# Kernel tuning notes

Measured on AMD Instinct MI355X. Metric: run time of the kernel, lower is better.

The kernel has to match this reference:

```python
import jax, jax.numpy as jnp
import numpy as np

EPS = 1e-5


def gcn_conv(x, W, b, src, dst, ew, num_nodes):
    """GCNConv with add_self_loops=True, symmetric normalization (PyG default)."""
    # degree at destination, self-loop weight 1.0 included implicitly
    deg = jax.ops.segment_sum(ew, dst, num_segments=num_nodes) + 1.0  # [N]
    dinv = jax.lax.rsqrt(deg)                                         # deg >= 1
    norm = dinv[src] * ew * dinv[dst]                                 # [E]
    h = x @ W                                                         # [N, F]
    msg = norm[:, None] * h[src]                                      # [E, F]
    agg = jax.ops.segment_sum(msg, dst, num_segments=num_nodes)       # [N, F]
    # self-loop contribution: dinv[i] * 1 * dinv[i] = 1/deg[i]
    agg = agg + h * (1.0 / deg)[:, None]
    return agg + b


def batchnorm(h, gamma, beta):
    mean = jnp.mean(h, axis=0)
    var = jnp.mean(jnp.square(h - mean), axis=0)  # biased, training-mode stats
    return (h - mean) * jax.lax.rsqrt(var + EPS) * gamma + beta


def setup_inputs() -> dict:
    key = jax.random.key(0)
    ks = jax.random.split(key, 8)
    N, E, F = 50000, 800000, 64
    x = jax.random.normal(ks[0], (N, F), dtype=jnp.float32)
    edge_index = jax.random.randint(ks[1], (2, E), 0, N, dtype=jnp.int64)
    edge_weight = jax.random.uniform(ks[2], (E,), dtype=jnp.float32)
    s = 1.0 / np.sqrt(F)
    W1 = jax.random.uniform(ks[3], (F, F), jnp.float32, -s, s)
    b1 = jnp.zeros((F,), jnp.float32)
    W2 = jax.random.uniform(ks[4], (F, F), jnp.float32, -s, s)
    b2 = jnp.zeros((F,), jnp.float32)
    gamma1 = jnp.ones((F,), jnp.float32)
    beta1 = jnp.zeros((F,), jnp.float32)
    gamma2 = jnp.ones((F,), jnp.float32)
    beta2 = jnp.zeros((F,), jnp.float32)
    return {"x": x, "edge_index": edge_index, "edge_weight": edge_weight,
            "W1": W1, "b1": b1, "gamma1": gamma1, "beta1": beta1,
            "W2": W2, "b2": b2, "gamma2": gamma2, "beta2": beta2}


def reference(x, edge_index, edge_weight, W1, b1, gamma1, beta1, W2, b2, gamma2, beta2):
    N = x.shape[0]
    src, dst = edge_index[0], edge_index[1]
    identity = x
    out = gcn_conv(x, W1, b1, src, dst, edge_weight, N)
    out = jax.nn.relu(batchnorm(out, gamma1, beta1))
    out = gcn_conv(out, W2, b2, src, dst, edge_weight, N)
    out = batchnorm(out, gamma2, beta2)
    out = out + identity  # residual: num_input_features == hidden_dim
    return jax.nn.relu(out)
```

## Files before the change

### kernel.cpp

```cpp
#include <hip/hip_runtime.h>
#include <math.h>

#define FEAT 64
#define BN_EPS 1e-5f
#define BN_REPS 64
#define CNT_REPS 4

__device__ __forceinline__ int edge_idx(const void* p, int is64, long long i) {
    return is64 ? (int)((const long long*)p)[i] : ((const int*)p)[i];
}

__device__ __forceinline__ float4 f4fma(float a, float4 b, float4 c) {
    return make_float4(fmaf(a, b.x, c.x), fmaf(a, b.y, c.y),
                       fmaf(a, b.z, c.z), fmaf(a, b.w, c.w));
}

__device__ __forceinline__ unsigned bf16rtne(float f) {
    unsigned u = __float_as_uint(f);
    return (u + 0x7fffu + ((u >> 16) & 1u)) >> 16;
}
__device__ __forceinline__ unsigned packbf2(float a, float b) {
    return bf16rtne(a) | (bf16rtne(b) << 16);
}
__device__ __forceinline__ float4 unpackbf4(uint2 r) {
    return make_float4(__uint_as_float(r.x << 16),
                       __uint_as_float(r.x & 0xffff0000u),
                       __uint_as_float(r.y << 16),
                       __uint_as_float(r.y & 0xffff0000u));
}

__global__ __launch_bounds__(256) void init_kernel(
    const unsigned* __restrict__ w, int* __restrict__ flag,
    int* __restrict__ cnt, float* __restrict__ parts, int N4) {
    int i = blockIdx.x * 256 + threadIdx.x;
    if (i < N4) cnt[i] = 0;
    if (blockIdx.x < 64) parts[blockIdx.x * 256 + threadIdx.x] = 0.0f;
    if (blockIdx.x == 0 && threadIdx.x < 64) {
        unsigned long long ok = __ballot(w[2 * threadIdx.x + 1] == 0u);
        if (threadIdx.x == 0) *flag = (ok == ~0ull);
    }
}

__global__ __launch_bounds__(256) void fused_count_gemm1_kernel(
    const void* __restrict__ ei, const int* __restrict__ flag,
    int* __restrict__ cnt, int* __restrict__ seq, int E,
    const float* __restrict__ x, const float* __restrict__ W1,
    uint2* __restrict__ out_bf, int N, int nc) {
    __shared__ float4 Ws4[64][16];
    __shared__ float xs[64][65];
    int tid = threadIdx.x;

    if ((int)blockIdx.x < nc) {
        int is64 = *flag;
        int T = nc * 256;
        int i = blockIdx.x * 256 + tid;
#pragma unroll
        for (int u = 0; u < 8; ++u) {
            int e = i + u * T;
            if (e < E) {
                int dst = edge_idx(ei, is64, (long long)E + e);
                seq[e] = atomicAdd(&cnt[(e & 3) * N + dst], 1);
            }
        }
        return;
    }

    int gb = blockIdx.x - nc;
    const float4* W4 = (const float4*)W1;
    for (int j = tid; j < 1024; j += 256) Ws4[j >> 4][j & 15] = W4[j];
    __syncthreads();

    int rowBase = gb * 64;
    for (int j = tid; j < 1024; j += 256) {
        int r = j >> 4, q = j & 15;
        int row = rowBase + r;
        float4 v = make_float4(0.f, 0.f, 0.f, 0.f);
        if (row < N) v = ((const float4*)x)[(size_t)row * 16 + q];
        xs[r][q * 4 + 0] = v.x;
        xs[r][q * 4 + 1] = v.y;
        xs[r][q * 4 + 2] = v.z;
        xs[r][q * 4 + 3] = v.w;
    }
    __syncthreads();

    int q = tid & 15, rg = tid >> 4;
    int r0 = rg * 4;
    float4 a0 = make_float4(0.f, 0.f, 0.f, 0.f), a1 = a0, a2 = a0, a3 = a0;
#pragma unroll 4
    for (int k = 0; k < 64; ++k) {
        float4 wv = Ws4[k][q];
        a0 = f4fma(xs[r0 + 0][k], wv, a0);
        a1 = f4fma(xs[r0 + 1][k], wv, a1);
        a2 = f4fma(xs[r0 + 2][k], wv, a2);
        a3 = f4fma(xs[r0 + 3][k], wv, a3);
    }
    int row = rowBase + r0;
    if (row + 0 < N) out_bf[(size_t)(row + 0) * 16 + q] = make_uint2(packbf2(a0.x, a0.y), packbf2(a0.z, a0.w));
    if (row + 1 < N) out_bf[(size_t)(row + 1) * 16 + q] = make_uint2(packbf2(a1.x, a1.y), packbf2(a1.z, a1.w));
    if (row + 2 < N) out_bf[(size_t)(row + 2) * 16 + q] = make_uint2(packbf2(a2.x, a2.y), packbf2(a2.z, a2.w));
    if (row + 3 < N) out_bf[(size_t)(row + 3) * 16 + q] = make_uint2(packbf2(a3.x, a3.y), packbf2(a3.z, a3.w));
}

__global__ __launch_bounds__(256) void scan1_kernel(const int* __restrict__ cnt,
                                                    int* __restrict__ excl,
                                                    int* __restrict__ bsum,
                                                    int N, int N4) {
    __shared__ int tmp[256];
    int j = blockIdx.x * 256 + threadIdx.x;
    int v = (j < N4) ? cnt[(j & 3) * N + (j >> 2)] : 0;
    tmp[threadIdx.x] = v;
    __syncthreads();
    for (int off = 1; off < 256; off <<= 1) {
        int t = (threadIdx.x >= off) ? tmp[threadIdx.x - off] : 0;
        __syncthreads();
        tmp[threadIdx.x] += t;
        __syncthreads();
    }
    if (j < N4) excl[j] = tmp[threadIdx.x] - v;
    if (threadIdx.x == 255) bsum[blockIdx.x] = tmp[255];
}

__global__ __launch_bounds__(256) void scan3_kernel(const int* __restrict__ excl,
                                                    const int* __restrict__ bsum,
                                                    int* __restrict__ rptrR,
                                                    int N4, int E, int nb) {
    __shared__ int red[256];
    int tid = threadIdx.x;
    int s = 0;
#pragma unroll
    for (int k = tid; k < 1024; k += 256)
        if (k < nb && k < (int)blockIdx.x) s += bsum[k];
    red[tid] = s;
    __syncthreads();
    for (int off = 128; off > 0; off >>= 1) {
        if (tid < off) red[tid] += red[tid + off];
        __syncthreads();
    }
    int base = red[0];
    int j = blockIdx.x * 256 + tid;
    if (j < N4) rptrR[j] = excl[j] + base;
    if (blockIdx.x == 0 && tid == 0) rptrR[N4] = E;
}

__global__ __launch_bounds__(256) void scatter_csr_kernel(
    const void* __restrict__ ei, const float* __restrict__ ew,
    const int* __restrict__ flag, const int* __restrict__ rptrR,
    const int* __restrict__ seq, unsigned* __restrict__ csr, int E) {
    int is64 = *flag;
    int T = gridDim.x * 256;
    int i = blockIdx.x * 256 + threadIdx.x;
#pragma unroll
    for (int u = 0; u < 2; ++u) {
        int e = i + u * T;
        if (e < E) {
            int src = edge_idx(ei, is64, e);
            int dst = edge_idx(ei, is64, (long long)E + e);
            int pos = rptrR[(dst << 2) | (e & 3)] + seq[e];
            csr[pos] = (unsigned)src | (bf16rtne(ew[e]) << 16);
        }
    }
}

__global__ __launch_bounds__(256) void deg_inv_kernel(
    const int* __restrict__ rptrR, const unsigned* __restrict__ csr,
    float* __restrict__ dinv, float* __restrict__ invdeg, int N) {
    int t = blockIdx.x * 256 + threadIdx.x;
    int n = t >> 3, l = t & 7;
    if (n >= N) return;
    int b = rptrR[n << 2], e = rptrR[(n << 2) + 4];
    float d = 0.0f;
    for (int k = b + l; k < e; k += 8)
        d += __uint_as_float(csr[k] & 0xffff0000u);
    d += __shfl_xor(d, 1);
    d += __shfl_xor(d, 2);
    d += __shfl_xor(d, 4);
    if (l == 0) {
        d += 1.0f;
        dinv[n]   = rsqrtf(d);
        invdeg[n] = 1.0f / d;
    }
}

__global__ __launch_bounds__(256) void fold_kernel(unsigned* __restrict__ csr,
                                                   const float* __restrict__ dinv,
                                                   int E) {
    int T = gridDim.x * 256;
    int i = blockIdx.x * 256 + threadIdx.x;
#pragma unroll
    for (int u = 0; u < 2; ++u) {
        int e = i + u * T;
        if (e < E) {
            unsigned v = csr[e];
            float nrm = dinv[v & 0xffffu] * __uint_as_float(v & 0xffff0000u);
            csr[e] = (v & 0xffffu) | (bf16rtne(nrm) << 16);
        }
    }
}

__global__ __launch_bounds__(256) void gemm2_kernel(
    const float* __restrict__ in, const float* __restrict__ W,
    const float* __restrict__ parts, const float* __restrict__ gamma,
    const float* __restrict__ beta, uint2* __restrict__ out_bf,
    int N, float invN) {
    __shared__ float4 Ws4[64][16];
    __shared__ float xs[64][65];
    __shared__ float sA[64], sS[64];
    int tid = threadIdx.x;
    const float4* W4 = (const float4*)W;
    for (int j = tid; j < 1024; j += 256) Ws4[j >> 4][j & 15] = W4[j];
    if (tid < 64) {
        float sm = 0.f, sq = 0.f;
#pragma unroll
        for (int r = 0; r < BN_REPS; ++r) {
            sm += parts[r * 128 + tid];
            sq += parts[r * 128 + 64 + tid];
        }
        float m = sm * invN;
        float var = fmaxf(sq * invN - m * m, 0.0f);
        float aa = gamma[tid] * rsqrtf(var + BN_EPS);
        sA[tid] = aa;
        sS[tid] = beta[tid] - m * aa;
    }
    __syncthreads();

    int rowBase = blockIdx.x * 64;
    for (int j = tid; j < 1024; j += 256) {
        int r = j >> 4, q = j & 15;
        int row = rowBase + r;
        float4 v = make_float4(0.f, 0.f, 0.f, 0.f);
        if (row < N) {
            v = ((const float4*)in)[(size_t)row * 16 + q];
            int c = q * 4;
            v.x = fmaxf(fmaf(v.x, sA[c + 0], sS[c + 0]), 0.f);
            v.y = fmaxf(fmaf(v.y, sA[c + 1], sS[c + 1]), 0.f);
            v.z = fmaxf(fmaf(v.z, sA[c + 2], sS[c + 2]), 0.f);
            v.w = fmaxf(fmaf(v.w, sA[c + 3], sS[c + 3]), 0.f);
        }
        xs[r][q * 4 + 0] = v.x;
        xs[r][q * 4 + 1] = v.y;
        xs[r][q * 4 + 2] = v.z;
        xs[r][q * 4 + 3] = v.w;
    }
    __syncthreads();

    int q = tid & 15, rg = tid >> 4;
    int r0 = rg * 4;
    float4 a0 = make_float4(0.f, 0.f, 0.f, 0.f), a1 = a0, a2 = a0, a3 = a0;
#pragma unroll 4
    for (int k = 0; k < 64; ++k) {
        float4 wv = Ws4[k][q];
        a0 = f4fma(xs[r0 + 0][k], wv, a0);
        a1 = f4fma(xs[r0 + 1][k], wv, a1);
        a2 = f4fma(xs[r0 + 2][k], wv, a2);
        a3 = f4fma(xs[r0 + 3][k], wv, a3);
    }
    int row = rowBase + r0;
    if (row + 0 < N) out_bf[(size_t)(row + 0) * 16 + q] = make_uint2(packbf2(a0.x, a0.y), packbf2(a0.z, a0.w));
    if (row + 1 < N) out_bf[(size_t)(row + 1) * 16 + q] = make_uint2(packbf2(a1.x, a1.y), packbf2(a1.z, a1.w));
    if (row + 2 < N) out_bf[(size_t)(row + 2) * 16 + q] = make_uint2(packbf2(a2.x, a2.y), packbf2(a2.z, a2.w));
    if (row + 3 < N) out_bf[(size_t)(row + 3) * 16 + q] = make_uint2(packbf2(a3.x, a3.y), packbf2(a3.z, a3.w));
}

__global__ __launch_bounds__(256) void gather_agg_kernel(
    const uint2* __restrict__ h2, const int* __restrict__ rptrR,
    const unsigned* __restrict__ csr, const float* __restrict__ dinv,
    const float* __restrict__ invdeg, const float* __restrict__ bias,
    float* __restrict__ agg, float* __restrict__ parts, int N) {
    int tid = threadIdx.x;
    int wave = tid >> 6, lane = tid & 63;
    int sub = lane >> 4, sl = lane & 15;
    float4 bv = ((const float4*)bias)[sl];
    float4 bnS = make_float4(0.f, 0.f, 0.f, 0.f), bnQ = bnS;

    int n0 = blockIdx.x * 16 + wave * 4;
#pragma unroll
    for (int i = 0; i < 4; ++i) {
        int n = n0 + i;
        if (n >= N) break;
        int beg = rptrR[n << 2], end = rptrR[(n << 2) + 4];
        uint2 selfr = h2[(size_t)n * 16 + sl];
        float dn = dinv[n], idg = invdeg[n];

        float4 accE = make_float4(0.f, 0.f, 0.f, 0.f);
        for (int k = beg; k < end; k += 32) {
            int srcs[8]; float w[8];
#pragma unroll
            for (int j = 0; j < 8; ++j) {
                int idx = k + sub + 4 * j;
                if (idx < end) {
                    unsigned v = __builtin_nontemporal_load(&csr[idx]);
                    srcs[j] = (int)(v & 0xffffu);
                    w[j] = __uint_as_float(v & 0xffff0000u);
                } else { srcs[j] = 0; w[j] = 0.f; }
            }
            uint2 hr[8];
#pragma unroll
            for (int j = 0; j < 8; ++j)
                hr[j] = (k + sub + 4 * j < end)
                          ? h2[(size_t)srcs[j] * 16 + sl] : make_uint2(0u, 0u);
#pragma unroll
            for (int j = 0; j < 8; ++j)
                accE = f4fma(w[j], unpackbf4(hr[j]), accE);
        }
        accE.x += __shfl_xor(accE.x, 16); accE.y += __shfl_xor(accE.y, 16);
        accE.z += __shfl_xor(accE.z, 16); accE.w += __shfl_xor(accE.w, 16);
        accE.x += __shfl_xor(accE.x, 32); accE.y += __shfl_xor(accE.y, 32);
        accE.z += __shfl_xor(accE.z, 32); accE.w += __shfl_xor(accE.w, 32);

        if (sub == 0) {
            float4 self = unpackbf4(selfr);
            float4 tot = f4fma(idg, self, bv);
            tot = f4fma(dn, accE, tot);
            ((float4*)agg)[(size_t)n * 16 + sl] = tot;
            bnS.x += tot.x; bnS.y += tot.y; bnS.z += tot.z; bnS.w += tot.w;
            bnQ.x = fmaf(tot.x, tot.x, bnQ.x); bnQ.y = fmaf(tot.y, tot.y, bnQ.y);
            bnQ.z = fmaf(tot.z, tot.z, bnQ.z); bnQ.w = fmaf(tot.w, tot.w, bnQ.w);
        }
    }

    __shared__ float4 LS[4][16], LQ[4][16];
    if (sub == 0) { LS[wave][sl] = bnS; LQ[wave][sl] = bnQ; }
    __syncthreads();
    if (tid < 16) {
        float4 ts = LS[0][tid], tq = LQ[0][tid];
        for (int i = 1; i < 4; ++i) {
            float4 a = LS[i][tid], b = LQ[i][tid];
            ts.x += a.x; ts.y += a.y; ts.z += a.z; ts.w += a.w;
            tq.x += b.x; tq.y += b.y; tq.z += b.z; tq.w += b.w;
        }
        float* P = parts + (size_t)(blockIdx.x & (BN_REPS - 1)) * 128;
        int c = tid * 4;
        unsafeAtomicAdd(&P[c + 0], ts.x);      unsafeAtomicAdd(&P[c + 1], ts.y);
        unsafeAtomicAdd(&P[c + 2], ts.z);      unsafeAtomicAdd(&P[c + 3], ts.w);
        unsafeAtomicAdd(&P[64 + c + 0], tq.x); unsafeAtomicAdd(&P[64 + c + 1], tq.y);
        unsafeAtomicAdd(&P[64 + c + 2], tq.z); unsafeAtomicAdd(&P[64 + c + 3], tq.w);
    }
}

__global__ __launch_bounds__(256) void final_out_kernel(
    const float* __restrict__ agg, const float* __restrict__ parts,
    const float* __restrict__ gamma, const float* __restrict__ beta,
    const float* __restrict__ x, float* __restrict__ out,
    int nquads, float invN) {
    __shared__ float sA[64], sS[64];
    int tid = threadIdx.x;
    if (tid < 64) {
        float sm = 0.f, sq = 0.f;
#pragma unroll
        for (int r = 0; r < BN_REPS; ++r) {
            sm += parts[r * 128 + tid];
            sq += parts[r * 128 + 64 + tid];
        }
        float m = sm * invN;
        float var = fmaxf(sq * invN - m * m, 0.0f);
        float aa = gamma[tid] * rsqrtf(var + BN_EPS);
        sA[tid] = aa;
        sS[tid] = beta[tid] - m * aa;
    }
    __syncthreads();
    int gid = blockIdx.x * 256 + tid;
    if (gid < nquads) {
        int c = (gid & 15) * 4;
        float4 g = ((const float4*)agg)[gid], xv = ((const float4*)x)[gid];
        float4 o;
        o.x = fmaxf(fmaf(g.x, sA[c + 0], sS[c + 0]) + xv.x, 0.f);
        o.y = fmaxf(fmaf(g.y, sA[c + 1], sS[c + 1]) + xv.y, 0.f);
        o.z = fmaxf(fmaf(g.z, sA[c + 2], sS[c + 2]) + xv.z, 0.f);
        o.w = fmaxf(fmaf(g.w, sA[c + 3], sS[c + 3]) + xv.w, 0.f);
        ((float4*)out)[gid] = o;
    }
}

extern "C" void kernel_launch(void* const* d_in, const int* in_sizes, int n_in,
                              void* d_out, int out_size, void* d_ws, size_t ws_size,
                              hipStream_t stream) {
    const float* x      = (const float*)d_in[0];
    const void*  ei     = d_in[1];
    const float* ew     = (const float*)d_in[2];
    const float* W1     = (const float*)d_in[3];
    const float* b1     = (const float*)d_in[4];
    const float* gamma1 = (const float*)d_in[5];
    const float* beta1  = (const float*)d_in[6];
    const float* W2     = (const float*)d_in[7];
    const float* b2     = (const float*)d_in[8];
    const float* gamma2 = (const float*)d_in[9];
    const float* beta2  = (const float*)d_in[10];
    float* out = (float*)d_out;

    const int N = in_sizes[0] / FEAT;
    const int E = in_sizes[2];
    const int N4 = N * CNT_REPS;

    char* ws = (char*)d_ws;
    size_t off = 0;
    auto alloc = [&](size_t bytes) {
        size_t o = off;
        off += (bytes + 255) & ~(size_t)255;
        return (void*)(ws + o);
    };
    int*      flag   = (int*)     alloc(256);
    int*      cnt    = (int*)     alloc((size_t)N4 * 4);
    int*      rptrR  = (int*)     alloc((size_t)(N4 + 1) * 4);
    int*      seq    = (int*)     alloc((size_t)E * 4);
    int*      excl   = (int*)     alloc((size_t)N4 * 4);
    int*      bsum   = (int*)     alloc(1024 * 4);
    float*    dinv   = (float*)   alloc((size_t)N * 4);
    float*    invdeg = (float*)   alloc((size_t)N * 4);
    float*    parts  = (float*)   alloc(2 * BN_REPS * 128 * 4);
    unsigned* csr    = (unsigned*)alloc((size_t)E * 4);
    uint2*    h_bf   = (uint2*)   alloc((size_t)N * 16 * 8);
    float*    agg    = (float*)   alloc((size_t)N * FEAT * 4);

    const int nblkN4 = (N4 + 255) / 256;
    const int nblkE2 = (E + 511) / 512;
    const int nblkQ  = (N * 16 + 255) / 256;
    const int nblkG  = (N + 63) / 64;
    const int nblkA  = (N + 15) / 16;
    const int nc     = (E + 2047) / 2048;
    const float invN = 1.0f / (float)N;

    init_kernel<<<nblkN4, 256, 0, stream>>>((const unsigned*)ei, flag, cnt, parts, N4);
    fused_count_gemm1_kernel<<<nc + nblkG, 256, 0, stream>>>(
        ei, flag, cnt, seq, E, x, W1, h_bf, N, nc);
    scan1_kernel<<<nblkN4, 256, 0, stream>>>(cnt, excl, bsum, N, N4);
    scan3_kernel<<<nblkN4, 256, 0, stream>>>(excl, bsum, rptrR, N4, E, nblkN4);
    scatter_csr_kernel<<<nblkE2, 256, 0, stream>>>(ei, ew, flag, rptrR, seq, csr, E);
    deg_inv_kernel<<<(N * 8 + 255) / 256, 256, 0, stream>>>(rptrR, csr, dinv, invdeg, N);
    fold_kernel<<<nblkE2, 256, 0, stream>>>(csr, dinv, E);

    gather_agg_kernel<<<nblkA, 256, 0, stream>>>(h_bf, rptrR, csr, dinv,
                                                 invdeg, b1, agg, parts, N);
    gemm2_kernel<<<nblkG, 256, 0, stream>>>(agg, W2, parts, gamma1, beta1,
                                            h_bf, N, invN);
    gather_agg_kernel<<<nblkA, 256, 0, stream>>>(h_bf, rptrR, csr, dinv,
                                                 invdeg, b2, agg,
                                                 parts + BN_REPS * 128, N);
    final_out_kernel<<<nblkQ, 256, 0, stream>>>(agg, parts + BN_REPS * 128,
                                                gamma2, beta2, x, out,
                                                N * 16, invN);
}
```

Baseline: 183.2 us.

## Drop fold kernel, apply source dinv in gather, store layer-1 aggregate as bf16

Removes the separate fold pass that rewrote each CSR weight with the source node's dinv. The gather now loads dinv[src] per edge and multiplies it in on the fly. The first gather also writes its aggregate as bf16 instead of fp32, and gemm2 reads that bf16 buffer, which halves that intermediate traffic. The trade-off is an extra random 4-byte load per edge in both gathers and lower precision on the layer-1 activations before batchnorm.

```diff
diff --git a/kernel.cpp b/kernel.cpp
--- a/kernel.cpp
+++ b/kernel.cpp
@@ -181,24 +181,8 @@
     }
 }
 
-__global__ __launch_bounds__(256) void fold_kernel(unsigned* __restrict__ csr,
-                                                   const float* __restrict__ dinv,
-                                                   int E) {
-    int T = gridDim.x * 256;
-    int i = blockIdx.x * 256 + threadIdx.x;
-#pragma unroll
-    for (int u = 0; u < 2; ++u) {
-        int e = i + u * T;
-        if (e < E) {
-            unsigned v = csr[e];
-            float nrm = dinv[v & 0xffffu] * __uint_as_float(v & 0xffff0000u);
-            csr[e] = (v & 0xffffu) | (bf16rtne(nrm) << 16);
-        }
-    }
-}
-
 __global__ __launch_bounds__(256) void gemm2_kernel(
-    const float* __restrict__ in, const float* __restrict__ W,
+    const uint2* __restrict__ in_bf, const float* __restrict__ W,
     const float* __restrict__ parts, const float* __restrict__ gamma,
     const float* __restrict__ beta, uint2* __restrict__ out_bf,
     int N, float invN) {
@@ -229,7 +213,7 @@
         int row = rowBase + r;
         float4 v = make_float4(0.f, 0.f, 0.f, 0.f);
         if (row < N) {
-            v = ((const float4*)in)[(size_t)row * 16 + q];
+            v = unpackbf4(in_bf[(size_t)row * 16 + q]);
             int c = q * 4;
             v.x = fmaxf(fmaf(v.x, sA[c + 0], sS[c + 0]), 0.f);
             v.y = fmaxf(fmaf(v.y, sA[c + 1], sS[c + 1]), 0.f);
@@ -261,11 +245,12 @@
     if (row + 3 < N) out_bf[(size_t)(row + 3) * 16 + q] = make_uint2(packbf2(a3.x, a3.y), packbf2(a3.z, a3.w));
 }
 
+template <int OBF>
 __global__ __launch_bounds__(256) void gather_agg_kernel(
     const uint2* __restrict__ h2, const int* __restrict__ rptrR,
     const unsigned* __restrict__ csr, const float* __restrict__ dinv,
     const float* __restrict__ invdeg, const float* __restrict__ bias,
-    float* __restrict__ agg, float* __restrict__ parts, int N) {
+    void* __restrict__ aggout, float* __restrict__ parts, int N) {
     int tid = threadIdx.x;
     int wave = tid >> 6, lane = tid & 63;
     int sub = lane >> 4, sl = lane & 15;
@@ -283,24 +268,29 @@
 
         float4 accE = make_float4(0.f, 0.f, 0.f, 0.f);
         for (int k = beg; k < end; k += 32) {
-            int srcs[8]; float w[8];
+            int srcs[8]; unsigned wraw[8];
 #pragma unroll
             for (int j = 0; j < 8; ++j) {
                 int idx = k + sub + 4 * j;
                 if (idx < end) {
                     unsigned v = __builtin_nontemporal_load(&csr[idx]);
                     srcs[j] = (int)(v & 0xffffu);
-                    w[j] = __uint_as_float(v & 0xffff0000u);
-                } else { srcs[j] = 0; w[j] = 0.f; }
+                    wraw[j] = v & 0xffff0000u;
+                } else { srcs[j] = 0; wraw[j] = 0u; }
             }
+            float dv[8];
             uint2 hr[8];
+#pragma unroll
+            for (int j = 0; j < 8; ++j)
+                dv[j] = dinv[srcs[j]];
 #pragma unroll
             for (int j = 0; j < 8; ++j)
                 hr[j] = (k + sub + 4 * j < end)
                           ? h2[(size_t)srcs[j] * 16 + sl] : make_uint2(0u, 0u);
 #pragma unroll
             for (int j = 0; j < 8; ++j)
-                accE = f4fma(w[j], unpackbf4(hr[j]), accE);
+                accE = f4fma(dv[j] * __uint_as_float(wraw[j]),
+                             unpackbf4(hr[j]), accE);
         }
         accE.x += __shfl_xor(accE.x, 16); accE.y += __shfl_xor(accE.y, 16);
         accE.z += __shfl_xor(accE.z, 16); accE.w += __shfl_xor(accE.w, 16);
@@ -311,7 +301,12 @@
             float4 self = unpackbf4(selfr);
             float4 tot = f4fma(idg, self, bv);
             tot = f4fma(dn, accE, tot);
-            ((float4*)agg)[(size_t)n * 16 + sl] = tot;
+            if (OBF) {
+                ((uint2*)aggout)[(size_t)n * 16 + sl] =
+                    make_uint2(packbf2(tot.x, tot.y), packbf2(tot.z, tot.w));
+            } else {
+                ((float4*)aggout)[(size_t)n * 16 + sl] = tot;
+            }
             bnS.x += tot.x; bnS.y += tot.y; bnS.z += tot.z; bnS.w += tot.w;
             bnQ.x = fmaf(tot.x, tot.x, bnQ.x); bnQ.y = fmaf(tot.y, tot.y, bnQ.y);
             bnQ.z = fmaf(tot.z, tot.z, bnQ.z); bnQ.w = fmaf(tot.w, tot.w, bnQ.w);
@@ -409,6 +404,7 @@
     float*    parts  = (float*)   alloc(2 * BN_REPS * 128 * 4);
     unsigned* csr    = (unsigned*)alloc((size_t)E * 4);
     uint2*    h_bf   = (uint2*)   alloc((size_t)N * 16 * 8);
+    uint2*    agg_bf = (uint2*)   alloc((size_t)N * 16 * 8);
     float*    agg    = (float*)   alloc((size_t)N * FEAT * 4);
 
     const int nblkN4 = (N4 + 255) / 256;
@@ -426,15 +422,14 @@
     scan3_kernel<<<nblkN4, 256, 0, stream>>>(excl, bsum, rptrR, N4, E, nblkN4);
     scatter_csr_kernel<<<nblkE2, 256, 0, stream>>>(ei, ew, flag, rptrR, seq, csr, E);
     deg_inv_kernel<<<(N * 8 + 255) / 256, 256, 0, stream>>>(rptrR, csr, dinv, invdeg, N);
-    fold_kernel<<<nblkE2, 256, 0, stream>>>(csr, dinv, E);
-
-    gather_agg_kernel<<<nblkA, 256, 0, stream>>>(h_bf, rptrR, csr, dinv,
-                                                 invdeg, b1, agg, parts, N);
-    gemm2_kernel<<<nblkG, 256, 0, stream>>>(agg, W2, parts, gamma1, beta1,
+
+    gather_agg_kernel<1><<<nblkA, 256, 0, stream>>>(h_bf, rptrR, csr, dinv,
+                                                    invdeg, b1, agg_bf, parts, N);
+    gemm2_kernel<<<nblkG, 256, 0, stream>>>(agg_bf, W2, parts, gamma1, beta1,
                                             h_bf, N, invN);
-    gather_agg_kernel<<<nblkA, 256, 0, stream>>>(h_bf, rptrR, csr, dinv,
-                                                 invdeg, b2, agg,
-                                                 parts + BN_REPS * 128, N);
+    gather_agg_kernel<0><<<nblkA, 256, 0, stream>>>(h_bf, rptrR, csr, dinv,
+                                                    invdeg, b2, agg,
+                                                    parts + BN_REPS * 128, N);
     final_out_kernel<<<nblkQ, 256, 0, stream>>>(agg, parts + BN_REPS * 128,
                                                 gamma2, beta2, x, out,
                                                 N * 16, invN);
```

After: 183.9 us. No clear change (+0.4%).
